# Optimization experiments

Hardware: AMD Instinct MI355X
Metric: run time of the kernel (lower is better)

The kernel has to match this reference:

```python
import jax, jax.numpy as jnp
import numpy as np

T, H, W = 16, 48, 48
C2D, C3D, DIM = 64, 64, 6
EPS = 1e-5


def _centered(s):
    # torch.linspace(-0.5*(s-1), 0.5*(s-1), s) == arange(s) - (s-1)/2
    return jnp.arange(s, dtype=jnp.float32) - 0.5 * (s - 1)


def _g_vol(t, h, w):
    grids = jnp.meshgrid(_centered(t), _centered(h), _centered(w), indexing='ij')
    return jnp.stack(grids, axis=-1).reshape(-1, 3)  # (Vs, 3)


def _g_slice(h, w):
    grids = jnp.meshgrid(_centered(1), _centered(h), _centered(w), indexing='ij')
    return jnp.stack(grids, axis=1)  # (1, 3, H, W)


def _layernorm(x, gamma, beta):
    mu = jnp.mean(x, axis=-1, keepdims=True)
    var = jnp.mean(jnp.square(x - mu), axis=-1, keepdims=True)
    return (x - mu) * jax.lax.rsqrt(var + EPS) * gamma + beta


def setup_inputs() -> dict:
    key = jax.random.key(0)
    ks = jax.random.split(key, 4)
    vol = jax.random.normal(ks[0], (1, C3D, T, H, W), dtype=jnp.float32)
    slc = jax.random.normal(ks[1], (1, C2D, H, W), dtype=jnp.float32)
    # proj weights ~ Normal(0, 1e-5) as in the torch module; biases zero
    w2d = jax.random.normal(ks[2], (DIM, C2D), dtype=jnp.float32) * 1e-5
    w3d = jax.random.normal(ks[3], (DIM, C3D), dtype=jnp.float32) * 1e-5
    return {
        'vol': vol, 'slc': slc,
        'w2d': w2d, 'b2d': jnp.zeros((DIM,), jnp.float32),
        'g2d': jnp.ones((DIM,), jnp.float32), 'be2d': jnp.zeros((DIM,), jnp.float32),
        'w3d': w3d, 'b3d': jnp.zeros((DIM,), jnp.float32),
        'g3d': jnp.ones((DIM,), jnp.float32), 'be3d': jnp.zeros((DIM,), jnp.float32),
    }


def reference(vol, slc, w2d, b2d, g2d, be2d, w3d, b3d, g3d, be3d):
    B, C, t, h, w = vol.shape
    Vs, Ss = t * h * w, h * w
    # ProjectLN2D: permute -> linear -> LN; flatten spatial to tokens
    q = _layernorm(jnp.einsum('bchw,dc->bhwd', slc, w2d) + b2d, g2d, be2d).reshape(B, Ss, -1)
    k = _layernorm(jnp.einsum('bcthw,dc->bthwd', vol, w3d) + b3d, g3d, be3d).reshape(B, Vs, -1)
    attn = jax.nn.softmax(jnp.einsum('bsd,bvd->bsv', q, k), axis=-1)  # (B, Ss, Vs)
    g_pred = jnp.einsum('bsv,vx->bsx', attn, _g_vol(t, h, w))  # (B, Ss, 3)
    flow = jnp.transpose(g_pred, (0, 2, 1)).reshape(B, 3, h, w) - _g_slice(h, w)
    return flow
```

## Files before the change

### kernel.cpp

```cpp
#include <hip/hip_runtime.h>
#include <math.h>

#define TT 16
#define HH 48
#define WW 48
#define CC 64
#define DD 6
#define VS (TT*HH*WW)
#define SS (HH*WW)
#define NT (VS/16)
#define QG 64
#define NQG (SS/QG)
#define NCH 32
#define TPC (NT/NCH)
#define LOG2E 1.44269504088896f

typedef float  f4 __attribute__((ext_vector_type(4)));
typedef float  f2 __attribute__((ext_vector_type(2)));
typedef _Float16 h4 __attribute__((ext_vector_type(4)));
typedef _Float16 h2 __attribute__((ext_vector_type(2)));

__global__ __launch_bounds__(256) void proj_kernel(
    const float* __restrict__ vol, const float* __restrict__ slc,
    const float* __restrict__ w2d, const float* __restrict__ b2d,
    const float* __restrict__ g2d, const float* __restrict__ be2d,
    const float* __restrict__ w3d, const float* __restrict__ b3d,
    const float* __restrict__ g3d, const float* __restrict__ be3d,
    f4* __restrict__ Kf, float* __restrict__ Qp)
{
    int tid = threadIdx.x;
    int gid = blockIdx.x * 256 + tid;
    __shared__ float sk[256][7];

    bool isK = gid < VS;
    const float *src, *wgt, *bia, *gam, *bet;
    int pos, stride;
    if (isK) { src = vol; wgt = w3d; bia = b3d; gam = g3d; bet = be3d; pos = gid;      stride = VS; }
    else     { src = slc; wgt = w2d; bia = b2d; gam = g2d; bet = be2d; pos = gid - VS; stride = SS; }

    float y[DD];
    {
        float acc[DD] = {0.f,0.f,0.f,0.f,0.f,0.f};
        for (int c = 0; c < CC; ++c) {
            float x = src[c * stride + pos];
            #pragma unroll
            for (int d = 0; d < DD; ++d) acc[d] = fmaf(wgt[d*CC + c], x, acc[d]);
        }
        float mu = 0.f;
        #pragma unroll
        for (int d = 0; d < DD; ++d) { acc[d] += bia[d]; mu += acc[d]; }
        mu *= (1.f/DD);
        float var = 0.f;
        #pragma unroll
        for (int d = 0; d < DD; ++d) { float t = acc[d] - mu; var = fmaf(t, t, var); }
        var *= (1.f/DD);
        float inv = rsqrtf(var + 1e-5f);
        #pragma unroll
        for (int d = 0; d < DD; ++d) y[d] = (acc[d] - mu) * inv * gam[d] + bet[d];
    }

    if (isK) {
        #pragma unroll
        for (int d = 0; d < DD; ++d) sk[tid][d] = y[d];
        __syncthreads();

        int tl = tid >> 4;
        int r  = tid & 15;
        int tileg = blockIdx.x * 16 + tl;
        #pragma unroll
        for (int g = 0; g < 4; ++g) {
            h4 kh = (h4){0,0,0,0};
            if (g == 0) {
                kh = (h4){ (_Float16)sk[tl*16+r][0], (_Float16)sk[tl*16+r][1],
                           (_Float16)sk[tl*16+r][2], (_Float16)sk[tl*16+r][3] };
            } else if (g == 1) {
                kh = (h4){ (_Float16)sk[tl*16+r][4], (_Float16)sk[tl*16+r][5],
                           (_Float16)0.f, (_Float16)0.f };
            }
            h4 gh = (h4){0,0,0,0};
            if (r < 4) {
                #pragma unroll
                for (int j = 0; j < 4; ++j) {
                    int v   = tileg*16 + g*4 + j;
                    int t   = v / (HH*WW);
                    int rem = v - t*(HH*WW);
                    int h   = rem / WW;
                    int w   = rem - h*WW;
                    float val = (r==0) ? (float)t - 7.5f
                              : (r==1) ? (float)h - 23.5f
                              : (r==2) ? (float)w - 23.5f
                              :          1.0f;
                    gh[j] = (_Float16)val;
                }
            }
            f2 kl = __builtin_bit_cast(f2, kh);
            f2 gl = __builtin_bit_cast(f2, gh);
            f4 o = (f4){kl.x, kl.y, gl.x, gl.y};
            Kf[tileg*64 + r + 16*g] = o;
        }
    } else {
        #pragma unroll
        for (int d = 0; d < DD; ++d) Qp[pos*8 + d] = y[d] * LOG2E;
        Qp[pos*8 + 6] = 0.f;
        Qp[pos*8 + 7] = 0.f;
    }
}

__global__ __launch_bounds__(256) void attn_kernel(
    const f4* __restrict__ Kf, const float* __restrict__ Qp,
    float* __restrict__ Pc)
{
    int tid  = threadIdx.x;
    int wv   = tid >> 6;
    int lane = tid & 63;
    int g = lane >> 4, r = lane & 15;
    int qg = blockIdx.x >> 5;
    int ch = blockIdx.x & (NCH-1);
    int qbase = qg*QG + wv*16;

    h4 qf = (h4){0,0,0,0};
    if (g < 2) {
        f4 qv = *(const f4*)(Qp + (qbase + r)*8 + g*4);
        qf = (h4){ (_Float16)qv.x, (_Float16)qv.y, (_Float16)qv.z, (_Float16)qv.w };
    }

    f4 z   = (f4){0,0,0,0};
    f4 out = (f4){0,0,0,0};
    const f4* kp = Kf + (ch*TPC)*64 + lane;
    #pragma unroll 4
    for (int it = 0; it < TPC; ++it) {
        f4 v = kp[it*64];
        h4 ka = __builtin_bit_cast(h4, (f2){v.x, v.y});
        h4 ga = __builtin_bit_cast(h4, (f2){v.z, v.w});
        f4 s = __builtin_amdgcn_mfma_f32_16x16x16f16(ka, qf, z, 0, 0, 0);
        float p0 = __builtin_amdgcn_exp2f(s.x);
        float p1 = __builtin_amdgcn_exp2f(s.y);
        float p2 = __builtin_amdgcn_exp2f(s.z);
        float p3 = __builtin_amdgcn_exp2f(s.w);
        h2 pl = __builtin_bit_cast(h2, __builtin_amdgcn_cvt_pkrtz(p0, p1));
        h2 ph = __builtin_bit_cast(h2, __builtin_amdgcn_cvt_pkrtz(p2, p3));
        h4 pf = (h4){pl.x, pl.y, ph.x, ph.y};
        out = __builtin_amdgcn_mfma_f32_16x16x16f16(pf, ga, out, 0, 0, 0);
    }
    if (r < 4) {
        #pragma unroll
        for (int j = 0; j < 4; ++j) {
            int q = qbase + g*4 + j;
            Pc[(ch*SS + q)*4 + r] = out[j];
        }
    }
}

__global__ __launch_bounds__(256) void final_kernel(
    const f4* __restrict__ Pc, float* __restrict__ out)
{
    int q = blockIdx.x * 256 + threadIdx.x;
    if (q >= SS) return;
    f4 a = (f4){0,0,0,0};
    #pragma unroll
    for (int c = 0; c < NCH; ++c) a += Pc[c*SS + q];
    float inv = 1.f / a.w;
    int h = q / WW;
    int w = q - h*WW;
    out[q]        = a.x * inv;
    out[SS + q]   = a.y * inv - ((float)h - 23.5f);
    out[2*SS + q] = a.z * inv - ((float)w - 23.5f);
}

extern "C" void kernel_launch(void* const* d_in, const int* in_sizes, int n_in,
                              void* d_out, int out_size, void* d_ws, size_t ws_size,
                              hipStream_t stream)
{
    const float* vol  = (const float*)d_in[0];
    const float* slc  = (const float*)d_in[1];
    const float* w2d  = (const float*)d_in[2];
    const float* b2d  = (const float*)d_in[3];
    const float* g2d  = (const float*)d_in[4];
    const float* be2d = (const float*)d_in[5];
    const float* w3d  = (const float*)d_in[6];
    const float* b3d  = (const float*)d_in[7];
    const float* g3d  = (const float*)d_in[8];
    const float* be3d = (const float*)d_in[9];
    float* out = (float*)d_out;

    f4*    Kf = (f4*)d_ws;
    float* Qp = (float*)(Kf + NT*64);
    f4*    Pc = (f4*)(Qp + SS*8);

    proj_kernel<<<(VS + SS)/256, 256, 0, stream>>>(vol, slc, w2d, b2d, g2d, be2d,
                                                   w3d, b3d, g3d, be3d, Kf, Qp);
    attn_kernel<<<NQG*NCH, 256, 0, stream>>>(Kf, Qp, (float*)Pc);
    final_kernel<<<(SS + 255)/256, 256, 0, stream>>>(Pc, out);
}
```

Before: 30.62 us.

## Process four query fragments per wave to reuse K loads across queries

The attention kernel now uses single-wave blocks that each handle 64 queries as four MFMA fragments. Each loaded K/grid tile is reused for all four fragments instead of being reloaded by four separate waves. The key dimension is split into 64 chunks instead of 32, which doubles the partial-sum buffer and the reduction work in the final kernel. The projection channel loop is also fully unrolled.

```diff
diff --git a/kernel.cpp b/kernel.cpp
--- a/kernel.cpp
+++ b/kernel.cpp
@@ -9,9 +9,10 @@
 #define VS (TT*HH*WW)
 #define SS (HH*WW)
 #define NT (VS/16)
-#define QG 64
-#define NQG (SS/QG)
-#define NCH 32
+#define QW 64
+#define NFR 4
+#define NQG (SS/QW)
+#define NCH 64
 #define TPC (NT/NCH)
 #define LOG2E 1.44269504088896f
 
@@ -41,6 +42,7 @@
     float y[DD];
     {
         float acc[DD] = {0.f,0.f,0.f,0.f,0.f,0.f};
+        #pragma unroll
         for (int c = 0; c < CC; ++c) {
             float x = src[c * stride + pos];
             #pragma unroll
@@ -106,48 +108,58 @@
     }
 }
 
-__global__ __launch_bounds__(256) void attn_kernel(
+__global__ __launch_bounds__(64, 4) void attn_kernel(
     const f4* __restrict__ Kf, const float* __restrict__ Qp,
     float* __restrict__ Pc)
 {
-    int tid  = threadIdx.x;
-    int wv   = tid >> 6;
-    int lane = tid & 63;
+    int lane = threadIdx.x;
     int g = lane >> 4, r = lane & 15;
-    int qg = blockIdx.x >> 5;
+    int qg = blockIdx.x >> 6;
     int ch = blockIdx.x & (NCH-1);
-    int qbase = qg*QG + wv*16;
-
-    h4 qf = (h4){0,0,0,0};
-    if (g < 2) {
-        f4 qv = *(const f4*)(Qp + (qbase + r)*8 + g*4);
-        qf = (h4){ (_Float16)qv.x, (_Float16)qv.y, (_Float16)qv.z, (_Float16)qv.w };
-    }
-
-    f4 z   = (f4){0,0,0,0};
-    f4 out = (f4){0,0,0,0};
+    int qbase = qg*QW;
+
+    h4 qf[NFR];
+    #pragma unroll
+    for (int f = 0; f < NFR; ++f) {
+        qf[f] = (h4){0,0,0,0};
+        if (g < 2) {
+            f4 qv = *(const f4*)(Qp + (qbase + f*16 + r)*8 + g*4);
+            qf[f] = (h4){ (_Float16)qv.x, (_Float16)qv.y, (_Float16)qv.z, (_Float16)qv.w };
+        }
+    }
+
+    f4 z = (f4){0,0,0,0};
+    f4 out[NFR];
+    #pragma unroll
+    for (int f = 0; f < NFR; ++f) out[f] = z;
+
     const f4* kp = Kf + (ch*TPC)*64 + lane;
-    #pragma unroll 4
+    #pragma unroll 2
     for (int it = 0; it < TPC; ++it) {
         f4 v = kp[it*64];
         h4 ka = __builtin_bit_cast(h4, (f2){v.x, v.y});
         h4 ga = __builtin_bit_cast(h4, (f2){v.z, v.w});
-        f4 s = __builtin_amdgcn_mfma_f32_16x16x16f16(ka, qf, z, 0, 0, 0);
-        float p0 = __builtin_amdgcn_exp2f(s.x);
-        float p1 = __builtin_amdgcn_exp2f(s.y);
-        float p2 = __builtin_amdgcn_exp2f(s.z);
-        float p3 = __builtin_amdgcn_exp2f(s.w);
-        h2 pl = __builtin_bit_cast(h2, __builtin_amdgcn_cvt_pkrtz(p0, p1));
-        h2 ph = __builtin_bit_cast(h2, __builtin_amdgcn_cvt_pkrtz(p2, p3));
-        h4 pf = (h4){pl.x, pl.y, ph.x, ph.y};
-        out = __builtin_amdgcn_mfma_f32_16x16x16f16(pf, ga, out, 0, 0, 0);
+        #pragma unroll
+        for (int f = 0; f < NFR; ++f) {
+            f4 s = __builtin_amdgcn_mfma_f32_16x16x16f16(ka, qf[f], z, 0, 0, 0);
+            float p0 = __builtin_amdgcn_exp2f(s.x);
+            float p1 = __builtin_amdgcn_exp2f(s.y);
+            float p2 = __builtin_amdgcn_exp2f(s.z);
+            float p3 = __builtin_amdgcn_exp2f(s.w);
+            h2 pl = __builtin_bit_cast(h2, __builtin_amdgcn_cvt_pkrtz(p0, p1));
+            h2 ph = __builtin_bit_cast(h2, __builtin_amdgcn_cvt_pkrtz(p2, p3));
+            h4 pf = (h4){pl.x, pl.y, ph.x, ph.y};
+            out[f] = __builtin_amdgcn_mfma_f32_16x16x16f16(pf, ga, out[f], 0, 0, 0);
+        }
     }
     if (r < 4) {
         #pragma unroll
-        for (int j = 0; j < 4; ++j) {
-            int q = qbase + g*4 + j;
-            Pc[(ch*SS + q)*4 + r] = out[j];
-        }
+        for (int f = 0; f < NFR; ++f)
+            #pragma unroll
+            for (int j = 0; j < 4; ++j) {
+                int q = qbase + f*16 + g*4 + j;
+                Pc[(ch*SS + q)*4 + r] = out[f][j];
+            }
     }
 }
 
@@ -157,7 +169,7 @@
     int q = blockIdx.x * 256 + threadIdx.x;
     if (q >= SS) return;
     f4 a = (f4){0,0,0,0};
-    #pragma unroll
+    #pragma unroll 8
     for (int c = 0; c < NCH; ++c) a += Pc[c*SS + q];
     float inv = 1.f / a.w;
     int h = q / WW;
@@ -189,6 +201,6 @@
 
     proj_kernel<<<(VS + SS)/256, 256, 0, stream>>>(vol, slc, w2d, b2d, g2d, be2d,
                                                    w3d, b3d, g3d, be3d, Kf, Qp);
-    attn_kernel<<<NQG*NCH, 256, 0, stream>>>(Kf, Qp, (float*)Pc);
+    attn_kernel<<<NQG*NCH, 64, 0, stream>>>(Kf, Qp, (float*)Pc);
     final_kernel<<<(SS + 255)/256, 256, 0, stream>>>(Pc, out);
 }
```

Measured after the change: 35.30 us. 1.15x slower.

## Switch attention to 32x32x16 MFMA tiles with register prefetch and wave-level reduction

Applied to the files above, without the earlier changes.

Restructures the attention kernel to use 32x32x16 f16 MFMA instead of 16x16x16, so each wave handles 32 queries against 32-key supertiles. Exp'd scores are repacked across half-waves with shuffles to form the B operand. K and grid data are laid out in a new 192-vector-per-supertile format, and the next tile's loads are software-prefetched. Query rows are stored directly as f16. Key chunks rise to 128, and the final reduction moves to a wave-per-query shuffle reduction over a query-major partial buffer. The aim is fewer MFMA issues and better load latency hiding, at the cost of the shuffle overhead and more partial sums to reduce.

```diff
diff --git a/kernel.cpp b/kernel.cpp
--- a/kernel.cpp
+++ b/kernel.cpp
@@ -8,17 +8,18 @@
 #define DD 6
 #define VS (TT*HH*WW)
 #define SS (HH*WW)
-#define NT (VS/16)
-#define QG 64
-#define NQG (SS/QG)
-#define NCH 32
-#define TPC (NT/NCH)
+#define NST (VS/32)
+#define NCH 128
+#define SPC (NST/NCH)
+#define QPB 128
+#define NQB (SS/QPB)
 #define LOG2E 1.44269504088896f
 
-typedef float  f4 __attribute__((ext_vector_type(4)));
-typedef float  f2 __attribute__((ext_vector_type(2)));
-typedef _Float16 h4 __attribute__((ext_vector_type(4)));
-typedef _Float16 h2 __attribute__((ext_vector_type(2)));
+typedef float    f4   __attribute__((ext_vector_type(4)));
+typedef float    f16v __attribute__((ext_vector_type(16)));
+typedef _Float16 h8   __attribute__((ext_vector_type(8)));
+typedef int      i4   __attribute__((ext_vector_type(4)));
+
 
 __global__ __launch_bounds__(256) void proj_kernel(
     const float* __restrict__ vol, const float* __restrict__ slc,
@@ -26,11 +27,10 @@
     const float* __restrict__ g2d, const float* __restrict__ be2d,
     const float* __restrict__ w3d, const float* __restrict__ b3d,
     const float* __restrict__ g3d, const float* __restrict__ be3d,
-    f4* __restrict__ Kf, float* __restrict__ Qp)
+    f4* __restrict__ Kf4, f4* __restrict__ Qh4)
 {
     int tid = threadIdx.x;
     int gid = blockIdx.x * 256 + tid;
-    __shared__ float sk[256][7];
 
     bool isK = gid < VS;
     const float *src, *wgt, *bia, *gam, *bet;
@@ -60,111 +60,133 @@
     }
 
     if (isK) {
-        #pragma unroll
-        for (int d = 0; d < DD; ++d) sk[tid][d] = y[d];
-        __syncthreads();
-
-        int tl = tid >> 4;
-        int r  = tid & 15;
-        int tileg = blockIdx.x * 16 + tl;
-        #pragma unroll
-        for (int g = 0; g < 4; ++g) {
-            h4 kh = (h4){0,0,0,0};
-            if (g == 0) {
-                kh = (h4){ (_Float16)sk[tl*16+r][0], (_Float16)sk[tl*16+r][1],
-                           (_Float16)sk[tl*16+r][2], (_Float16)sk[tl*16+r][3] };
-            } else if (g == 1) {
-                kh = (h4){ (_Float16)sk[tl*16+r][4], (_Float16)sk[tl*16+r][5],
-                           (_Float16)0.f, (_Float16)0.f };
-            }
-            h4 gh = (h4){0,0,0,0};
-            if (r < 4) {
+        int stl = tid >> 5, r = tid & 31;
+        int stg = blockIdx.x * 8 + stl;
+        h8 kh = (h8){ (_Float16)y[0], (_Float16)y[1], (_Float16)y[2],
+                      (_Float16)y[3], (_Float16)y[4], (_Float16)y[5],
+                      (_Float16)0.f, (_Float16)0.f };
+        Kf4[(size_t)stg*192 + r]      = __builtin_bit_cast(f4, kh);
+        Kf4[(size_t)stg*192 + 32 + r] = (f4){0.f,0.f,0.f,0.f};
+
+        for (int s = tid; s < 1024; s += 256) {
+            int ss  = s >> 7;
+            int rem = s & 127;
+            int w   = rem >> 6;
+            int l   = rem & 63;
+            int h   = l >> 5, c = l & 31;
+            h8 gh = (h8){0,0,0,0,0,0,0,0};
+            if (c < 4) {
+                int vb = (blockIdx.x*8 + ss)*32 + w*16 + h*8;
                 #pragma unroll
-                for (int j = 0; j < 4; ++j) {
-                    int v   = tileg*16 + g*4 + j;
-                    int t   = v / (HH*WW);
-                    int rem = v - t*(HH*WW);
-                    int h   = rem / WW;
-                    int w   = rem - h*WW;
-                    float val = (r==0) ? (float)t - 7.5f
-                              : (r==1) ? (float)h - 23.5f
-                              : (r==2) ? (float)w - 23.5f
+                for (int j = 0; j < 8; ++j) {
+                    int v  = vb + j;
+                    int t  = v / (HH*WW);
+                    int rm = v - t*(HH*WW);
+                    int hh = rm / WW;
+                    int ww = rm - hh*WW;
+                    float val = (c==0) ? (float)t - 7.5f
+                              : (c==1) ? (float)hh - 23.5f
+                              : (c==2) ? (float)ww - 23.5f
                               :          1.0f;
                     gh[j] = (_Float16)val;
                 }
             }
-            f2 kl = __builtin_bit_cast(f2, kh);
-            f2 gl = __builtin_bit_cast(f2, gh);
-            f4 o = (f4){kl.x, kl.y, gl.x, gl.y};
-            Kf[tileg*64 + r + 16*g] = o;
+            Kf4[(size_t)(blockIdx.x*8 + ss)*192 + 64 + w*64 + l] = __builtin_bit_cast(f4, gh);
         }
     } else {
-        #pragma unroll
-        for (int d = 0; d < DD; ++d) Qp[pos*8 + d] = y[d] * LOG2E;
-        Qp[pos*8 + 6] = 0.f;
-        Qp[pos*8 + 7] = 0.f;
+        h8 qh = (h8){ (_Float16)(y[0]*LOG2E), (_Float16)(y[1]*LOG2E),
+                      (_Float16)(y[2]*LOG2E), (_Float16)(y[3]*LOG2E),
+                      (_Float16)(y[4]*LOG2E), (_Float16)(y[5]*LOG2E),
+                      (_Float16)0.f, (_Float16)0.f };
+        Qh4[pos] = __builtin_bit_cast(f4, qh);
     }
 }
 
 __global__ __launch_bounds__(256) void attn_kernel(
-    const f4* __restrict__ Kf, const float* __restrict__ Qp,
-    float* __restrict__ Pc)
+    const f4* __restrict__ Kf4, const f4* __restrict__ Qh4,
+    f4* __restrict__ Pc4)
 {
     int tid  = threadIdx.x;
     int wv   = tid >> 6;
     int lane = tid & 63;
-    int g = lane >> 4, r = lane & 15;
-    int qg = blockIdx.x >> 5;
-    int ch = blockIdx.x & (NCH-1);
-    int qbase = qg*QG + wv*16;
-
-    h4 qf = (h4){0,0,0,0};
-    if (g < 2) {
-        f4 qv = *(const f4*)(Qp + (qbase + r)*8 + g*4);
-        qf = (h4){ (_Float16)qv.x, (_Float16)qv.y, (_Float16)qv.z, (_Float16)qv.w };
-    }
-
-    f4 z   = (f4){0,0,0,0};
-    f4 out = (f4){0,0,0,0};
-    const f4* kp = Kf + (ch*TPC)*64 + lane;
-    #pragma unroll 4
-    for (int it = 0; it < TPC; ++it) {
-        f4 v = kp[it*64];
-        h4 ka = __builtin_bit_cast(h4, (f2){v.x, v.y});
-        h4 ga = __builtin_bit_cast(h4, (f2){v.z, v.w});
-        f4 s = __builtin_amdgcn_mfma_f32_16x16x16f16(ka, qf, z, 0, 0, 0);
-        float p0 = __builtin_amdgcn_exp2f(s.x);
-        float p1 = __builtin_amdgcn_exp2f(s.y);
-        float p2 = __builtin_amdgcn_exp2f(s.z);
-        float p3 = __builtin_amdgcn_exp2f(s.w);
-        h2 pl = __builtin_bit_cast(h2, __builtin_amdgcn_cvt_pkrtz(p0, p1));
-        h2 ph = __builtin_bit_cast(h2, __builtin_amdgcn_cvt_pkrtz(p2, p3));
-        h4 pf = (h4){pl.x, pl.y, ph.x, ph.y};
-        out = __builtin_amdgcn_mfma_f32_16x16x16f16(pf, ga, out, 0, 0, 0);
-    }
-    if (r < 4) {
-        #pragma unroll
-        for (int j = 0; j < 4; ++j) {
-            int q = qbase + g*4 + j;
-            Pc[(ch*SS + q)*4 + r] = out[j];
-        }
+    int q31  = lane & 31;
+    bool lo  = lane < 32;
+    int qb   = blockIdx.x / NCH;
+    int ch   = blockIdx.x - qb*NCH;
+    int qbase = qb*QPB + wv*32;
+
+    f4 qv = (f4){0.f,0.f,0.f,0.f};
+    if (lo) qv = Qh4[qbase + q31];
+    h8 qf = __builtin_bit_cast(h8, qv);
+
+    f16v acc = {};
+    const f4* kp = Kf4 + (size_t)ch*SPC*192 + lane;
+
+    f4 va = kp[0], g0 = kp[64], g1 = kp[128];
+    for (int it = 0; it < SPC; ++it) {
+        f4 vaN, g0N, g1N;
+        if (it + 1 < SPC) {
+            const f4* kn = kp + (it+1)*192;
+            vaN = kn[0]; g0N = kn[64]; g1N = kn[128];
+        }
+        f16v s = __builtin_amdgcn_mfma_f32_32x32x16_f16(
+                     __builtin_bit_cast(h8, va), qf, (f16v){}, 0, 0, 0);
+        float p[16];
+        #pragma unroll
+        for (int r = 0; r < 16; ++r) p[r] = __builtin_amdgcn_exp2f(s[r]);
+        int U[8];
+        #pragma unroll
+        for (int m = 0; m < 4; ++m) {
+            U[2*m]   = __builtin_bit_cast(int, __builtin_amdgcn_cvt_pkrtz(p[4*m],   p[4*m+1]));
+            U[2*m+1] = __builtin_bit_cast(int, __builtin_amdgcn_cvt_pkrtz(p[4*m+2], p[4*m+3]));
+        }
+        #pragma unroll
+        for (int w = 0; w < 2; ++w) {
+            int a0 = U[4*w+0], a1 = U[4*w+1];
+            int b0 = U[4*w+2], b1 = U[4*w+3];
+            int a0s = __shfl_xor(a0, 32), b0s = __shfl_xor(b0, 32);
+            int a1s = __shfl_xor(a1, 32), b1s = __shfl_xor(b1, 32);
+            i4 pi;
+            pi.x = lo ? a0  : b0s;
+            pi.y = lo ? a1  : b1s;
+            pi.z = lo ? a0s : b0;
+            pi.w = lo ? a1s : b1;
+            h8 pf = __builtin_bit_cast(h8, pi);
+            h8 gf = __builtin_bit_cast(h8, (w == 0) ? g0 : g1);
+            acc = __builtin_amdgcn_mfma_f32_32x32x16_f16(gf, pf, acc, 0, 0, 0);
+        }
+        va = vaN; g0 = g0N; g1 = g1N;
+    }
+    if (lo) {
+        f4 o = (f4){acc[0], acc[1], acc[2], acc[3]};
+        Pc4[(size_t)(qbase + q31)*NCH + ch] = o;
     }
 }
 
 __global__ __launch_bounds__(256) void final_kernel(
-    const f4* __restrict__ Pc, float* __restrict__ out)
-{
-    int q = blockIdx.x * 256 + threadIdx.x;
-    if (q >= SS) return;
-    f4 a = (f4){0,0,0,0};
+    const f4* __restrict__ Pc4, float* __restrict__ out)
+{
+    int wv   = threadIdx.x >> 6;
+    int lane = threadIdx.x & 63;
+    int q = blockIdx.x * 4 + wv;
+
+    f4 a = Pc4[(size_t)q*NCH + lane] + Pc4[(size_t)q*NCH + 64 + lane];
+
     #pragma unroll
-    for (int c = 0; c < NCH; ++c) a += Pc[c*SS + q];
-    float inv = 1.f / a.w;
-    int h = q / WW;
-    int w = q - h*WW;
-    out[q]        = a.x * inv;
-    out[SS + q]   = a.y * inv - ((float)h - 23.5f);
-    out[2*SS + q] = a.z * inv - ((float)w - 23.5f);
+    for (int off = 32; off >= 1; off >>= 1) {
+        a.x += __shfl_xor(a.x, off);
+        a.y += __shfl_xor(a.y, off);
+        a.z += __shfl_xor(a.z, off);
+        a.w += __shfl_xor(a.w, off);
+    }
+    if (lane == 0) {
+        float inv = 1.f / a.w;
+        int h = q / WW;
+        int w = q - h*WW;
+        out[q]        = a.x * inv;
+        out[SS + q]   = a.y * inv - ((float)h - 23.5f);
+        out[2*SS + q] = a.z * inv - ((float)w - 23.5f);
+    }
 }
 
 extern "C" void kernel_launch(void* const* d_in, const int* in_sizes, int n_in,
@@ -183,12 +205,12 @@
     const float* be3d = (const float*)d_in[9];
     float* out = (float*)d_out;
 
-    f4*    Kf = (f4*)d_ws;
-    float* Qp = (float*)(Kf + NT*64);
-    f4*    Pc = (f4*)(Qp + SS*8);
+    f4* Kf4 = (f4*)d_ws;
+    f4* Qh4 = Kf4 + (size_t)NST*192;
+    f4* Pc4 = Qh4 + SS;
 
     proj_kernel<<<(VS + SS)/256, 256, 0, stream>>>(vol, slc, w2d, b2d, g2d, be2d,
-                                                   w3d, b3d, g3d, be3d, Kf, Qp);
-    attn_kernel<<<NQG*NCH, 256, 0, stream>>>(Kf, Qp, (float*)Pc);
-    final_kernel<<<(SS + 255)/256, 256, 0, stream>>>(Pc, out);
-}
+                                                   w3d, b3d, g3d, be3d, Kf4, Qh4);
+    attn_kernel<<<NQB*NCH, 256, 0, stream>>>(Kf4, Qh4, Pc4);
+    final_kernel<<<SS/4, 256, 0, stream>>>(Pc4, out);
+}
```

Measured after the change: 35.70 us. +16.6%, slower.
